# Performance work log

Measured on AMD Instinct MI355X. Metric: run time of the kernel, lower is better.

Reference implementation:

```python
import jax, jax.numpy as jnp
import numpy as np

DIM_QK = 1024


def setup_inputs() -> dict:
    key = jax.random.key(0)
    ks = jax.random.split(key, 5)
    B, S, D = 4, 2048, 1024
    return {
        "x": jax.random.normal(ks[0], (B, S, D), dtype=jnp.float32),
        "Wq": jax.random.normal(ks[1], (DIM_QK, D), dtype=jnp.float32) * (D ** -0.5),
        "Wk": jax.random.normal(ks[2], (DIM_QK, D), dtype=jnp.float32) * (D ** -0.5),
        "Wv": jax.random.normal(ks[3], (D, D), dtype=jnp.float32) * (D ** -0.5),
        "Wo": jax.random.normal(ks[4], (D, D), dtype=jnp.float32) * (D ** -0.5),
    }


def reference(x, Wq, Wk, Wv, Wo):
    # torch Linear: y = x @ W.T (no bias)
    q = jnp.einsum('bsd,kd->bsk', x, Wq)
    k = jnp.einsum('bsd,kd->bsk', x, Wk)
    v = jnp.einsum('bsd,vd->bsv', x, Wv)
    scale = (DIM_QK // 2) ** (-0.5)
    dist = jnp.einsum('bqk,btk->bqt', q, k) * scale  # [B,S,S]
    weight = jax.lax.stop_gradient(dist)             # pre-softmax scores (detached)
    attn = jax.nn.softmax(dist, axis=-1)
    ctx = jnp.einsum('bqt,btv->bqv', attn, v)
    out = jnp.einsum('bqv,ev->bqe', ctx, Wo)
    return (out, weight)
```

## Files before the change

kernel.cpp:

```cpp
#include <hip/hip_runtime.h>
#include <stdint.h>

typedef __attribute__((ext_vector_type(8))) short bf16x8;
typedef __attribute__((ext_vector_type(4))) float f32x4;

__device__ __forceinline__ unsigned short f32_to_bf16(float f) {
  union { float f; unsigned int u; } v; v.f = f;
  unsigned int u = v.u;
  u += 0x7fffu + ((u >> 16) & 1u);
  return (unsigned short)(u >> 16);
}

__device__ __forceinline__ void gload_lds16(const unsigned short* g, unsigned short* lds) {
  __builtin_amdgcn_global_load_lds(
      (const __attribute__((address_space(1))) unsigned int*)g,
      (__attribute__((address_space(3))) unsigned int*)lds,
      16, 0, 0);
}

template<int MODE>
__global__ __launch_bounds__(256, 2)
void gemm_bt(const unsigned short* __restrict__ A,
             const unsigned short* __restrict__ Bm,
             void* __restrict__ Cv,
             int M, int N, int K, int lda, int ldb, int ldc,
             long sA_, long sB_, long sC_,
             float scale)
{
  __shared__ unsigned short sA[2 * 128 * 32];
  __shared__ unsigned short sB[2 * 128 * 32];

  const int bz = blockIdx.z;
  const unsigned short* Ab = A + (long)bz * sA_;
  const unsigned short* Bb = Bm + (long)bz * sB_;

  const int m0 = blockIdx.x * 128;
  const int n0 = blockIdx.y * 128;

  const int t = threadIdx.x;
  const int lane = t & 63;
  const int w = t >> 6;
  const int wr = (w >> 1) * 64;
  const int wc = (w & 1) * 64;

  f32x4 acc[4][4];
#pragma unroll
  for (int i = 0; i < 4; ++i)
#pragma unroll
    for (int j = 0; j < 4; ++j)
      acc[i][j] = (f32x4){0.f, 0.f, 0.f, 0.f};

  const int r0 = t >> 2;
  const int kc = (t & 3) * 8;
  const unsigned short* Ap0 = Ab + (long)(m0 + r0) * lda + kc;
  const unsigned short* Ap1 = Ab + (long)(m0 + r0 + 64) * lda + kc;
  const unsigned short* Bp0 = Bb + (long)(n0 + r0) * ldb + kc;
  const unsigned short* Bp1 = Bb + (long)(n0 + r0 + 64) * ldb + kc;

  const int lrow = lane & 15;
  const int q8 = (lane >> 4) * 8;

  for (int k0 = 0; k0 < K; k0 += 64) {
    __syncthreads();
    gload_lds16(Ap0 + k0,      &sA[t * 8]);
    gload_lds16(Ap1 + k0,      &sA[t * 8 + 2048]);
    gload_lds16(Ap0 + k0 + 32, &sA[4096 + t * 8]);
    gload_lds16(Ap1 + k0 + 32, &sA[4096 + t * 8 + 2048]);
    gload_lds16(Bp0 + k0,      &sB[t * 8]);
    gload_lds16(Bp1 + k0,      &sB[t * 8 + 2048]);
    gload_lds16(Bp0 + k0 + 32, &sB[4096 + t * 8]);
    gload_lds16(Bp1 + k0 + 32, &sB[4096 + t * 8 + 2048]);
    __syncthreads();

#pragma unroll
    for (int s = 0; s < 2; ++s) {
      bf16x8 af[4], bfr[4];
#pragma unroll
      for (int i = 0; i < 4; ++i) {
        af[i]  = *(const bf16x8*)&sA[s * 4096 + (wr + i * 16 + lrow) * 32 + q8];
        bfr[i] = *(const bf16x8*)&sB[s * 4096 + (wc + i * 16 + lrow) * 32 + q8];
      }
#pragma unroll
      for (int mi = 0; mi < 4; ++mi)
#pragma unroll
        for (int ni = 0; ni < 4; ++ni)
          acc[mi][ni] = __builtin_amdgcn_mfma_f32_16x16x32_bf16(af[mi], bfr[ni], acc[mi][ni], 0, 0, 0);
    }
  }

  const int cl = lane & 15;
  const int rq = (lane >> 4) * 4;

  if (MODE == 2) {
    float* Cb = (float*)Cv + (long)bz * sC_;
#pragma unroll
    for (int mi = 0; mi < 4; ++mi) {
      const int rowb = m0 + wr + mi * 16 + rq;
#pragma unroll
      for (int ni = 0; ni < 4; ++ni) {
        const int col = n0 + wc + ni * 16 + cl;
#pragma unroll
        for (int r = 0; r < 4; ++r)
          Cb[(long)(rowb + r) * ldc + col] = acc[mi][ni][r] * scale;
      }
    }
  } else {
    unsigned short* Cb = (unsigned short*)Cv + (long)bz * sC_;
#pragma unroll
    for (int mi = 0; mi < 4; ++mi) {
      const int rowb = m0 + wr + mi * 16 + rq;
#pragma unroll
      for (int ni = 0; ni < 4; ++ni) {
        const int col = n0 + wc + ni * 16 + cl;
#pragma unroll
        for (int r = 0; r < 4; ++r)
          Cb[(long)(rowb + r) * ldc + col] = f32_to_bf16(acc[mi][ni][r]);
      }
    }
  }
}

__global__ __launch_bounds__(256)
void softmax_rows(const float* __restrict__ dist, unsigned short* __restrict__ attn) {
  const long row = blockIdx.x;
  const float4* in = (const float4*)(dist + row * 2048);
  const int t = threadIdx.x;
  float4 v0 = in[t];
  float4 v1 = in[t + 256];

  float m = fmaxf(fmaxf(fmaxf(v0.x, v0.y), fmaxf(v0.z, v0.w)),
                  fmaxf(fmaxf(v1.x, v1.y), fmaxf(v1.z, v1.w)));
#pragma unroll
  for (int off = 32; off > 0; off >>= 1)
    m = fmaxf(m, __shfl_xor(m, off, 64));

  __shared__ float redm[4];
  __shared__ float reds[4];
  if ((t & 63) == 0) redm[t >> 6] = m;
  __syncthreads();
  m = fmaxf(fmaxf(redm[0], redm[1]), fmaxf(redm[2], redm[3]));

  float e[8];
  e[0] = __expf(v0.x - m); e[1] = __expf(v0.y - m);
  e[2] = __expf(v0.z - m); e[3] = __expf(v0.w - m);
  e[4] = __expf(v1.x - m); e[5] = __expf(v1.y - m);
  e[6] = __expf(v1.z - m); e[7] = __expf(v1.w - m);

  float s = ((e[0] + e[1]) + (e[2] + e[3])) + ((e[4] + e[5]) + (e[6] + e[7]));
#pragma unroll
  for (int off = 32; off > 0; off >>= 1)
    s += __shfl_xor(s, off, 64);
  if ((t & 63) == 0) reds[t >> 6] = s;
  __syncthreads();
  s = (reds[0] + reds[1]) + (reds[2] + reds[3]);

  const float inv = 1.0f / s;
  ushort4 o0, o1;
  o0.x = f32_to_bf16(e[0] * inv); o0.y = f32_to_bf16(e[1] * inv);
  o0.z = f32_to_bf16(e[2] * inv); o0.w = f32_to_bf16(e[3] * inv);
  o1.x = f32_to_bf16(e[4] * inv); o1.y = f32_to_bf16(e[5] * inv);
  o1.z = f32_to_bf16(e[6] * inv); o1.w = f32_to_bf16(e[7] * inv);
  *(ushort4*)(attn + row * 2048 + t * 4) = o0;
  *(ushort4*)(attn + row * 2048 + 1024 + t * 4) = o1;
}

__global__ __launch_bounds__(256)
void cast_all(const float* __restrict__ Wq, const float* __restrict__ Wk,
              const float* __restrict__ Wv, const float* __restrict__ Wo,
              const float* __restrict__ x, unsigned short* __restrict__ dst) {
  const long i = ((long)blockIdx.x * 256 + threadIdx.x) * 4;
  const float* src;
  long off;
  if (i < 4194304) {
    const int which = (int)(i >> 20);
    src = (which == 0) ? Wq : (which == 1) ? Wk : (which == 2) ? Wv : Wo;
    off = i & 1048575;
  } else {
    src = x;
    off = i - 4194304;
  }
  float4 v = *(const float4*)(src + off);
  ushort4 o;
  o.x = f32_to_bf16(v.x); o.y = f32_to_bf16(v.y);
  o.z = f32_to_bf16(v.z); o.w = f32_to_bf16(v.w);
  *(ushort4*)(dst + i) = o;
}

extern "C" void kernel_launch(void* const* d_in, const int* in_sizes, int n_in,
                              void* d_out, int out_size, void* d_ws, size_t ws_size,
                              hipStream_t stream) {
  const float* x  = (const float*)d_in[0];
  const float* Wq = (const float*)d_in[1];
  const float* Wk = (const float*)d_in[2];
  const float* Wv = (const float*)d_in[3];
  const float* Wo = (const float*)d_in[4];

  const long Bn = 4, S = 2048, D = 1024;
  const long MS = Bn * S;

  float* out_p  = (float*)d_out;
  float* weight = out_p + MS * D;

  unsigned short* Wqb = (unsigned short*)d_ws;
  unsigned short* Wvb = Wqb + 2 * D * D;
  unsigned short* Wob = Wvb + D * D;
  unsigned short* xb  = Wob + D * D;
  unsigned short* qk  = xb + MS * D;
  unsigned short* vtb = qk + MS * 2048;
  unsigned short* attn = qk;
  unsigned short* ctx  = xb;

  cast_all<<<12288, 256, 0, stream>>>(Wq, Wk, Wv, Wo, x, Wqb);

  gemm_bt<0><<<dim3(64, 16, 1), 256, 0, stream>>>(xb, Wqb, qk, 8192, 2048, 1024,
                                                  1024, 1024, 2048, 0, 0, 0, 1.f);
  gemm_bt<0><<<dim3(8, 16, 4), 256, 0, stream>>>(Wvb, xb, vtb, 1024, 2048, 1024,
                                                 1024, 1024, 2048, 0, S * D, D * S, 1.f);
  gemm_bt<2><<<dim3(16, 16, 4), 256, 0, stream>>>(qk, qk + 1024, weight, 2048, 2048, 1024,
                                                  2048, 2048, 2048,
                                                  S * 2048, S * 2048, S * S,
                                                  0.04419417382415922f);
  softmax_rows<<<(int)(Bn * S), 256, 0, stream>>>(weight, attn);
  gemm_bt<0><<<dim3(16, 8, 4), 256, 0, stream>>>(attn, vtb, ctx, 2048, 1024, 2048,
                                                 2048, 2048, 1024,
                                                 S * S, D * S, S * D, 1.f);
  gemm_bt<2><<<dim3(64, 8, 1), 256, 0, stream>>>(ctx, Wob, out_p, 8192, 1024, 1024,
                                                 1024, 1024, 1024, 0, 0, 0, 1.f);
}
```

Before: 319.7 us.

## Rewrite GEMM as 256x256-tile, 512-thread kernel with software-pipelined LDS prefetch

Replaces the 128x128 double-sync GEMM with a 256x256 tile computed by 8 waves. Global-to-LDS loads for the next k-tiles are issued in the middle of the MFMA phases across a 128KB double buffer, with explicit vmcnt waits and raised wave priority around the MFMAs. The larger tiles improve operand reuse, and the prefetch is meant to hide load latency behind compute. In exchange, the large LDS footprint and 32 accumulators per lane reduce occupancy, and some GEMMs now launch only 128-256 blocks.

```diff
diff --git a/kernel.cpp b/kernel.cpp
--- a/kernel.cpp
+++ b/kernel.cpp
@@ -11,15 +11,63 @@
   return (unsigned short)(u >> 16);
 }
 
-__device__ __forceinline__ void gload_lds16(const unsigned short* g, unsigned short* lds) {
+__device__ __forceinline__ void gload_lds16(const unsigned short* g, unsigned short* lds_p) {
   __builtin_amdgcn_global_load_lds(
       (const __attribute__((address_space(1))) unsigned int*)g,
-      (__attribute__((address_space(3))) unsigned int*)lds,
+      (__attribute__((address_space(3))) unsigned int*)lds_p,
       16, 0, 0);
 }
 
+
+#define VM8  asm volatile("s_waitcnt vmcnt(8)" ::: "memory")
+#define VM4  asm volatile("s_waitcnt vmcnt(4)" ::: "memory")
+#define VM0_ asm volatile("s_waitcnt vmcnt(0)" ::: "memory")
+#define VMNO ((void)0)
+
+#define ISSUE_A(KT, KK) do {                                                  \
+    const unsigned short* ga_ = As0 + (KT) * 64 + (KK) * 32;                  \
+    unsigned short* la_ = &lds[(((KT) & 1) << 15) + (KK) * 8192 + t * 8];     \
+    gload_lds16(ga_, la_);                                                    \
+    gload_lds16(ga_ + a128, la_ + 4096);                                      \
+  } while (0)
+
+#define ISSUE_B(KT, KK) do {                                                  \
+    const unsigned short* gb_ = Bs0 + (KT) * 64 + (KK) * 32;                  \
+    unsigned short* lb_ = &lds[(((KT) & 1) << 15) + 16384 + (KK) * 8192 + t * 8]; \
+    gload_lds16(gb_, lb_);                                                    \
+    gload_lds16(gb_ + b128, lb_ + 4096);                                      \
+  } while (0)
+
+#define PH(BUFB, KK, MH, LOADB, ISSUE_CODE, VMC) do {                         \
+    const int ab_ = (BUFB) + (KK) * 8192;                                     \
+    if (LOADB) {                                                              \
+      const int bb2_ = (BUFB) + 16384 + (KK) * 8192;                          \
+      _Pragma("unroll")                                                       \
+      for (int ni_ = 0; ni_ < 4; ++ni_)                                       \
+        bfr[ni_] = *(const bf16x8*)&lds[bb2_ + (wc + ni_ * 16 + lrow) * 32 + q8e]; \
+    }                                                                         \
+    bf16x8 af_[4];                                                            \
+    _Pragma("unroll")                                                         \
+    for (int mi_ = 0; mi_ < 4; ++mi_)                                         \
+      af_[mi_] = *(const bf16x8*)&lds[ab_ + (wr + (MH) * 64 + mi_ * 16 + lrow) * 32 + q8e]; \
+    ISSUE_CODE;                                                               \
+    __builtin_amdgcn_s_setprio(1);                                            \
+    _Pragma("unroll")                                                         \
+    for (int mi_ = 0; mi_ < 4; ++mi_) {                                       \
+      _Pragma("unroll")                                                       \
+      for (int ni_ = 0; ni_ < 4; ++ni_)                                       \
+        acc[(MH) * 4 + mi_][ni_] = __builtin_amdgcn_mfma_f32_16x16x32_bf16(   \
+            af_[mi_], bfr[ni_], acc[(MH) * 4 + mi_][ni_], 0, 0, 0);           \
+    }                                                                         \
+    __builtin_amdgcn_s_setprio(0);                                            \
+    VMC;                                                                      \
+    asm volatile("s_waitcnt lgkmcnt(0)" ::: "memory");                        \
+    __builtin_amdgcn_s_barrier();                                             \
+    asm volatile("" ::: "memory");                                            \
+  } while (0)
+
 template<int MODE>
-__global__ __launch_bounds__(256, 2)
+__global__ __launch_bounds__(512, 2)
 void gemm_bt(const unsigned short* __restrict__ A,
              const unsigned short* __restrict__ Bm,
              void* __restrict__ Cv,
@@ -27,65 +75,69 @@
              long sA_, long sB_, long sC_,
              float scale)
 {
-  __shared__ unsigned short sA[2 * 128 * 32];
-  __shared__ unsigned short sB[2 * 128 * 32];
+  __shared__ unsigned short lds[65536];
 
   const int bz = blockIdx.z;
   const unsigned short* Ab = A + (long)bz * sA_;
   const unsigned short* Bb = Bm + (long)bz * sB_;
 
-  const int m0 = blockIdx.x * 128;
-  const int n0 = blockIdx.y * 128;
+  const int m0 = blockIdx.x * 256;
+  const int n0 = blockIdx.y * 256;
 
   const int t = threadIdx.x;
   const int lane = t & 63;
   const int w = t >> 6;
-  const int wr = (w >> 1) * 64;
-  const int wc = (w & 1) * 64;
-
-  f32x4 acc[4][4];
-#pragma unroll
-  for (int i = 0; i < 4; ++i)
+  const int wr = (w >> 2) * 128;
+  const int wc = (w & 3) * 64;
+  const int lrow = lane & 15;
+  const int q8e = (lane >> 4) * 8;
+
+  const int row0 = t >> 2;
+  const int kc0 = (t & 3) * 8;
+  const unsigned short* As0 = Ab + (long)(m0 + row0) * lda + kc0;
+  const unsigned short* Bs0 = Bb + (long)(n0 + row0) * ldb + kc0;
+  const long a128 = (long)lda * 128;
+  const long b128 = (long)ldb * 128;
+
+  f32x4 acc[8][4];
+#pragma unroll
+  for (int i = 0; i < 8; ++i)
 #pragma unroll
     for (int j = 0; j < 4; ++j)
       acc[i][j] = (f32x4){0.f, 0.f, 0.f, 0.f};
 
-  const int r0 = t >> 2;
-  const int kc = (t & 3) * 8;
-  const unsigned short* Ap0 = Ab + (long)(m0 + r0) * lda + kc;
-  const unsigned short* Ap1 = Ab + (long)(m0 + r0 + 64) * lda + kc;
-  const unsigned short* Bp0 = Bb + (long)(n0 + r0) * ldb + kc;
-  const unsigned short* Bp1 = Bb + (long)(n0 + r0 + 64) * ldb + kc;
-
-  const int lrow = lane & 15;
-  const int q8 = (lane >> 4) * 8;
-
-  for (int k0 = 0; k0 < K; k0 += 64) {
-    __syncthreads();
-    gload_lds16(Ap0 + k0,      &sA[t * 8]);
-    gload_lds16(Ap1 + k0,      &sA[t * 8 + 2048]);
-    gload_lds16(Ap0 + k0 + 32, &sA[4096 + t * 8]);
-    gload_lds16(Ap1 + k0 + 32, &sA[4096 + t * 8 + 2048]);
-    gload_lds16(Bp0 + k0,      &sB[t * 8]);
-    gload_lds16(Bp1 + k0,      &sB[t * 8 + 2048]);
-    gload_lds16(Bp0 + k0 + 32, &sB[4096 + t * 8]);
-    gload_lds16(Bp1 + k0 + 32, &sB[4096 + t * 8 + 2048]);
-    __syncthreads();
-
-#pragma unroll
-    for (int s = 0; s < 2; ++s) {
-      bf16x8 af[4], bfr[4];
-#pragma unroll
-      for (int i = 0; i < 4; ++i) {
-        af[i]  = *(const bf16x8*)&sA[s * 4096 + (wr + i * 16 + lrow) * 32 + q8];
-        bfr[i] = *(const bf16x8*)&sB[s * 4096 + (wc + i * 16 + lrow) * 32 + q8];
-      }
-#pragma unroll
-      for (int mi = 0; mi < 4; ++mi)
-#pragma unroll
-        for (int ni = 0; ni < 4; ++ni)
-          acc[mi][ni] = __builtin_amdgcn_mfma_f32_16x16x32_bf16(af[mi], bfr[ni], acc[mi][ni], 0, 0, 0);
-    }
+  const int NT = K >> 6;
+
+  ISSUE_A(0, 0); ISSUE_B(0, 0);
+  ISSUE_A(0, 1); ISSUE_B(0, 1);
+  ISSUE_A(1, 0); ISSUE_B(1, 0);
+  VM8;
+  __builtin_amdgcn_s_barrier();
+  asm volatile("" ::: "memory");
+
+  bf16x8 bfr[4];
+  int kt = 0;
+  for (; kt < NT - 2; ++kt) {
+    const int bb = (kt & 1) << 15;
+    PH(bb, 0, 0, 1, ISSUE_A(kt + 1, 1), VMNO);
+    PH(bb, 0, 1, 0, ISSUE_B(kt + 1, 1), VM8);
+    PH(bb, 1, 0, 1, ISSUE_A(kt + 2, 0), VMNO);
+    PH(bb, 1, 1, 0, ISSUE_B(kt + 2, 0), VM8);
+  }
+  {
+    const int bb = (kt & 1) << 15;
+    PH(bb, 0, 0, 1, ISSUE_A(kt + 1, 1), VMNO);
+    PH(bb, 0, 1, 0, ISSUE_B(kt + 1, 1), VM8);
+    PH(bb, 1, 0, 1, VMNO, VMNO);
+    PH(bb, 1, 1, 0, VMNO, VM4);
+    ++kt;
+  }
+  {
+    const int bb = (kt & 1) << 15;
+    PH(bb, 0, 0, 1, VMNO, VMNO);
+    PH(bb, 0, 1, 0, VMNO, VM0_);
+    PH(bb, 1, 0, 1, VMNO, VMNO);
+    PH(bb, 1, 1, 0, VMNO, VMNO);
   }
 
   const int cl = lane & 15;
@@ -94,27 +146,27 @@
   if (MODE == 2) {
     float* Cb = (float*)Cv + (long)bz * sC_;
 #pragma unroll
-    for (int mi = 0; mi < 4; ++mi) {
-      const int rowb = m0 + wr + mi * 16 + rq;
+    for (int mig = 0; mig < 8; ++mig) {
+      const int rowb = m0 + wr + (mig >> 2) * 64 + (mig & 3) * 16 + rq;
 #pragma unroll
       for (int ni = 0; ni < 4; ++ni) {
         const int col = n0 + wc + ni * 16 + cl;
 #pragma unroll
         for (int r = 0; r < 4; ++r)
-          Cb[(long)(rowb + r) * ldc + col] = acc[mi][ni][r] * scale;
+          Cb[(long)(rowb + r) * ldc + col] = acc[mig][ni][r] * scale;
       }
     }
   } else {
     unsigned short* Cb = (unsigned short*)Cv + (long)bz * sC_;
 #pragma unroll
-    for (int mi = 0; mi < 4; ++mi) {
-      const int rowb = m0 + wr + mi * 16 + rq;
+    for (int mig = 0; mig < 8; ++mig) {
+      const int rowb = m0 + wr + (mig >> 2) * 64 + (mig & 3) * 16 + rq;
 #pragma unroll
       for (int ni = 0; ni < 4; ++ni) {
         const int col = n0 + wc + ni * 16 + cl;
 #pragma unroll
         for (int r = 0; r < 4; ++r)
-          Cb[(long)(rowb + r) * ldc + col] = f32_to_bf16(acc[mi][ni][r]);
+          Cb[(long)(rowb + r) * ldc + col] = f32_to_bf16(acc[mig][ni][r]);
       }
     }
   }
@@ -212,18 +264,18 @@
 
   cast_all<<<12288, 256, 0, stream>>>(Wq, Wk, Wv, Wo, x, Wqb);
 
-  gemm_bt<0><<<dim3(64, 16, 1), 256, 0, stream>>>(xb, Wqb, qk, 8192, 2048, 1024,
-                                                  1024, 1024, 2048, 0, 0, 0, 1.f);
-  gemm_bt<0><<<dim3(8, 16, 4), 256, 0, stream>>>(Wvb, xb, vtb, 1024, 2048, 1024,
-                                                 1024, 1024, 2048, 0, S * D, D * S, 1.f);
-  gemm_bt<2><<<dim3(16, 16, 4), 256, 0, stream>>>(qk, qk + 1024, weight, 2048, 2048, 1024,
-                                                  2048, 2048, 2048,
-                                                  S * 2048, S * 2048, S * S,
-                                                  0.04419417382415922f);
+  gemm_bt<0><<<dim3(32, 8, 1), 512, 0, stream>>>(xb, Wqb, qk, 8192, 2048, 1024,
+                                                 1024, 1024, 2048, 0, 0, 0, 1.f);
+  gemm_bt<0><<<dim3(4, 8, 4), 512, 0, stream>>>(Wvb, xb, vtb, 1024, 2048, 1024,
+                                                1024, 1024, 2048, 0, S * D, D * S, 1.f);
+  gemm_bt<2><<<dim3(8, 8, 4), 512, 0, stream>>>(qk, qk + 1024, weight, 2048, 2048, 1024,
+                                                2048, 2048, 2048,
+                                                S * 2048, S * 2048, S * S,
+                                                0.04419417382415922f);
   softmax_rows<<<(int)(Bn * S), 256, 0, stream>>>(weight, attn);
-  gemm_bt<0><<<dim3(16, 8, 4), 256, 0, stream>>>(attn, vtb, ctx, 2048, 1024, 2048,
-                                                 2048, 2048, 1024,
-                                                 S * S, D * S, S * D, 1.f);
-  gemm_bt<2><<<dim3(64, 8, 1), 256, 0, stream>>>(ctx, Wob, out_p, 8192, 1024, 1024,
+  gemm_bt<0><<<dim3(8, 4, 4), 512, 0, stream>>>(attn, vtb, ctx, 2048, 1024, 2048,
+                                                2048, 2048, 1024,
+                                                S * S, D * S, S * D, 1.f);
+  gemm_bt<2><<<dim3(32, 4, 1), 512, 0, stream>>>(ctx, Wob, out_p, 8192, 1024, 1024,
                                                  1024, 1024, 1024, 0, 0, 0, 1.f);
 }
```

After: 346.9 us. 8.5% more time.

## Swizzle LDS tiles, add 128x256 GEMM tile, merge V projection into one GEMM

Applied to the files above, without the earlier changes.

Stores the A and B tiles in LDS with an XOR-swizzled k-chunk index (row-dependent), and reads them back with the matching swizzle. The aim is to cut bank conflicts on the 16-byte fragment reads feeding the MFMAs. A new gemm_a kernel with a 128x256 block tile and 4x8 accumulators per wave is used for the Q/K projection and the QK^T score GEMM, raising operand reuse per LDS load at the cost of more accumulator registers and fewer blocks. The V^T projection becomes a single non-batched GEMM producing a 1024x8192 layout, and the attn@V GEMM reads it with an adjusted stride.

```diff
diff --git a/kernel.cpp b/kernel.cpp
--- a/kernel.cpp
+++ b/kernel.cpp
@@ -11,21 +11,125 @@
   return (unsigned short)(u >> 16);
 }
 
-__device__ __forceinline__ void gload_lds16(const unsigned short* g, unsigned short* lds) {
+__device__ __forceinline__ void gload_lds16(const unsigned short* g, unsigned short* lds_p) {
   __builtin_amdgcn_global_load_lds(
       (const __attribute__((address_space(1))) unsigned int*)g,
-      (__attribute__((address_space(3))) unsigned int*)lds,
+      (__attribute__((address_space(3))) unsigned int*)lds_p,
       16, 0, 0);
 }
+
 
 template<int MODE>
 __global__ __launch_bounds__(256, 2)
-void gemm_bt(const unsigned short* __restrict__ A,
-             const unsigned short* __restrict__ Bm,
-             void* __restrict__ Cv,
-             int M, int N, int K, int lda, int ldb, int ldc,
-             long sA_, long sB_, long sC_,
-             float scale)
+void gemm_a(const unsigned short* __restrict__ A,
+            const unsigned short* __restrict__ Bm,
+            void* __restrict__ Cv,
+            int M, int N, int K, int lda, int ldb, int ldc,
+            long sA_, long sB_, long sC_,
+            float scale)
+{
+  __shared__ unsigned short sA[2 * 128 * 32];
+  __shared__ unsigned short sB[2 * 256 * 32];
+
+  const int bz = blockIdx.z;
+  const unsigned short* Ab = A + (long)bz * sA_;
+  const unsigned short* Bb = Bm + (long)bz * sB_;
+
+  const int m0 = blockIdx.x * 128;
+  const int n0 = blockIdx.y * 256;
+
+  const int t = threadIdx.x;
+  const int lane = t & 63;
+  const int w = t >> 6;
+  const int wr = (w >> 1) * 64;
+  const int wc = (w & 1) * 128;
+  const int lrow = lane & 15;
+  const int q8s = ((lane >> 4) ^ ((lrow >> 1) & 3)) * 8;
+
+  const int row0 = t >> 2;
+  const int kc0 = ((t & 3) ^ ((t >> 3) & 3)) * 8;
+  const unsigned short* Ap = Ab + (long)(m0 + row0) * lda + kc0;
+  const unsigned short* Bp = Bb + (long)(n0 + row0) * ldb + kc0;
+  const long a64 = (long)lda * 64;
+  const long b64 = (long)ldb * 64;
+
+  f32x4 acc[4][8];
+#pragma unroll
+  for (int i = 0; i < 4; ++i)
+#pragma unroll
+    for (int j = 0; j < 8; ++j)
+      acc[i][j] = (f32x4){0.f, 0.f, 0.f, 0.f};
+
+  for (int k0 = 0; k0 < K; k0 += 64) {
+    __syncthreads();
+#pragma unroll
+    for (int s = 0; s < 2; ++s) {
+      const int gk = k0 + s * 32;
+      gload_lds16(Ap + gk,       &sA[s * 4096 + t * 8]);
+      gload_lds16(Ap + a64 + gk, &sA[s * 4096 + t * 8 + 2048]);
+#pragma unroll
+      for (int j = 0; j < 4; ++j)
+        gload_lds16(Bp + j * b64 + gk, &sB[s * 8192 + t * 8 + j * 2048]);
+    }
+    __syncthreads();
+
+#pragma unroll
+    for (int s = 0; s < 2; ++s) {
+      bf16x8 af[4], bf[8];
+#pragma unroll
+      for (int i = 0; i < 4; ++i)
+        af[i] = *(const bf16x8*)&sA[s * 4096 + (wr + i * 16 + lrow) * 32 + q8s];
+#pragma unroll
+      for (int n = 0; n < 8; ++n)
+        bf[n] = *(const bf16x8*)&sB[s * 8192 + (wc + n * 16 + lrow) * 32 + q8s];
+#pragma unroll
+      for (int mi = 0; mi < 4; ++mi)
+#pragma unroll
+        for (int ni = 0; ni < 8; ++ni)
+          acc[mi][ni] = __builtin_amdgcn_mfma_f32_16x16x32_bf16(af[mi], bf[ni], acc[mi][ni], 0, 0, 0);
+    }
+  }
+
+  const int cl = lane & 15;
+  const int rq = (lane >> 4) * 4;
+
+  if (MODE == 2) {
+    float* Cb = (float*)Cv + (long)bz * sC_;
+#pragma unroll
+    for (int mi = 0; mi < 4; ++mi) {
+      const int rowb = m0 + wr + mi * 16 + rq;
+#pragma unroll
+      for (int ni = 0; ni < 8; ++ni) {
+        const int col = n0 + wc + ni * 16 + cl;
+#pragma unroll
+        for (int r = 0; r < 4; ++r)
+          Cb[(long)(rowb + r) * ldc + col] = acc[mi][ni][r] * scale;
+      }
+    }
+  } else {
+    unsigned short* Cb = (unsigned short*)Cv + (long)bz * sC_;
+#pragma unroll
+    for (int mi = 0; mi < 4; ++mi) {
+      const int rowb = m0 + wr + mi * 16 + rq;
+#pragma unroll
+      for (int ni = 0; ni < 8; ++ni) {
+        const int col = n0 + wc + ni * 16 + cl;
+#pragma unroll
+        for (int r = 0; r < 4; ++r)
+          Cb[(long)(rowb + r) * ldc + col] = f32_to_bf16(acc[mi][ni][r]);
+      }
+    }
+  }
+}
+
+template<int MODE>
+__global__ __launch_bounds__(256, 2)
+void gemm_b(const unsigned short* __restrict__ A,
+            const unsigned short* __restrict__ Bm,
+            void* __restrict__ Cv,
+            int M, int N, int K, int lda, int ldb, int ldc,
+            long sA_, long sB_, long sC_,
+            float scale)
 {
   __shared__ unsigned short sA[2 * 128 * 32];
   __shared__ unsigned short sB[2 * 128 * 32];
@@ -42,6 +146,15 @@
   const int w = t >> 6;
   const int wr = (w >> 1) * 64;
   const int wc = (w & 1) * 64;
+  const int lrow = lane & 15;
+  const int q8s = ((lane >> 4) ^ ((lrow >> 1) & 3)) * 8;
+
+  const int row0 = t >> 2;
+  const int kc0 = ((t & 3) ^ ((t >> 3) & 3)) * 8;
+  const unsigned short* Ap = Ab + (long)(m0 + row0) * lda + kc0;
+  const unsigned short* Bp = Bb + (long)(n0 + row0) * ldb + kc0;
+  const long a64 = (long)lda * 64;
+  const long b64 = (long)ldb * 64;
 
   f32x4 acc[4][4];
 #pragma unroll
@@ -50,41 +163,31 @@
     for (int j = 0; j < 4; ++j)
       acc[i][j] = (f32x4){0.f, 0.f, 0.f, 0.f};
 
-  const int r0 = t >> 2;
-  const int kc = (t & 3) * 8;
-  const unsigned short* Ap0 = Ab + (long)(m0 + r0) * lda + kc;
-  const unsigned short* Ap1 = Ab + (long)(m0 + r0 + 64) * lda + kc;
-  const unsigned short* Bp0 = Bb + (long)(n0 + r0) * ldb + kc;
-  const unsigned short* Bp1 = Bb + (long)(n0 + r0 + 64) * ldb + kc;
-
-  const int lrow = lane & 15;
-  const int q8 = (lane >> 4) * 8;
-
   for (int k0 = 0; k0 < K; k0 += 64) {
     __syncthreads();
-    gload_lds16(Ap0 + k0,      &sA[t * 8]);
-    gload_lds16(Ap1 + k0,      &sA[t * 8 + 2048]);
-    gload_lds16(Ap0 + k0 + 32, &sA[4096 + t * 8]);
-    gload_lds16(Ap1 + k0 + 32, &sA[4096 + t * 8 + 2048]);
-    gload_lds16(Bp0 + k0,      &sB[t * 8]);
-    gload_lds16(Bp1 + k0,      &sB[t * 8 + 2048]);
-    gload_lds16(Bp0 + k0 + 32, &sB[4096 + t * 8]);
-    gload_lds16(Bp1 + k0 + 32, &sB[4096 + t * 8 + 2048]);
+#pragma unroll
+    for (int s = 0; s < 2; ++s) {
+      const int gk = k0 + s * 32;
+      gload_lds16(Ap + gk,       &sA[s * 4096 + t * 8]);
+      gload_lds16(Ap + a64 + gk, &sA[s * 4096 + t * 8 + 2048]);
+      gload_lds16(Bp + gk,       &sB[s * 4096 + t * 8]);
+      gload_lds16(Bp + b64 + gk, &sB[s * 4096 + t * 8 + 2048]);
+    }
     __syncthreads();
 
 #pragma unroll
     for (int s = 0; s < 2; ++s) {
-      bf16x8 af[4], bfr[4];
+      bf16x8 af[4], bf[4];
 #pragma unroll
       for (int i = 0; i < 4; ++i) {
-        af[i]  = *(const bf16x8*)&sA[s * 4096 + (wr + i * 16 + lrow) * 32 + q8];
-        bfr[i] = *(const bf16x8*)&sB[s * 4096 + (wc + i * 16 + lrow) * 32 + q8];
+        af[i] = *(const bf16x8*)&sA[s * 4096 + (wr + i * 16 + lrow) * 32 + q8s];
+        bf[i] = *(const bf16x8*)&sB[s * 4096 + (wc + i * 16 + lrow) * 32 + q8s];
       }
 #pragma unroll
       for (int mi = 0; mi < 4; ++mi)
 #pragma unroll
         for (int ni = 0; ni < 4; ++ni)
-          acc[mi][ni] = __builtin_amdgcn_mfma_f32_16x16x32_bf16(af[mi], bfr[ni], acc[mi][ni], 0, 0, 0);
+          acc[mi][ni] = __builtin_amdgcn_mfma_f32_16x16x32_bf16(af[mi], bf[ni], acc[mi][ni], 0, 0, 0);
     }
   }
 
@@ -212,18 +315,18 @@
 
   cast_all<<<12288, 256, 0, stream>>>(Wq, Wk, Wv, Wo, x, Wqb);
 
-  gemm_bt<0><<<dim3(64, 16, 1), 256, 0, stream>>>(xb, Wqb, qk, 8192, 2048, 1024,
-                                                  1024, 1024, 2048, 0, 0, 0, 1.f);
-  gemm_bt<0><<<dim3(8, 16, 4), 256, 0, stream>>>(Wvb, xb, vtb, 1024, 2048, 1024,
-                                                 1024, 1024, 2048, 0, S * D, D * S, 1.f);
-  gemm_bt<2><<<dim3(16, 16, 4), 256, 0, stream>>>(qk, qk + 1024, weight, 2048, 2048, 1024,
-                                                  2048, 2048, 2048,
-                                                  S * 2048, S * 2048, S * S,
-                                                  0.04419417382415922f);
+  gemm_a<0><<<dim3(64, 8, 1), 256, 0, stream>>>(xb, Wqb, qk, 8192, 2048, 1024,
+                                                1024, 1024, 2048, 0, 0, 0, 1.f);
+  gemm_b<0><<<dim3(8, 64, 1), 256, 0, stream>>>(Wvb, xb, vtb, 1024, 8192, 1024,
+                                                1024, 1024, 8192, 0, 0, 0, 1.f);
+  gemm_a<2><<<dim3(16, 8, 4), 256, 0, stream>>>(qk, qk + 1024, weight, 2048, 2048, 1024,
+                                                2048, 2048, 2048,
+                                                S * 2048, S * 2048, S * S,
+                                                0.04419417382415922f);
   softmax_rows<<<(int)(Bn * S), 256, 0, stream>>>(weight, attn);
-  gemm_bt<0><<<dim3(16, 8, 4), 256, 0, stream>>>(attn, vtb, ctx, 2048, 1024, 2048,
-                                                 2048, 2048, 1024,
-                                                 S * S, D * S, S * D, 1.f);
-  gemm_bt<2><<<dim3(64, 8, 1), 256, 0, stream>>>(ctx, Wob, out_p, 8192, 1024, 1024,
-                                                 1024, 1024, 1024, 0, 0, 0, 1.f);
-}
+  gemm_b<0><<<dim3(16, 8, 4), 256, 0, stream>>>(attn, vtb, ctx, 2048, 1024, 2048,
+                                                2048, 8192, 1024,
+                                                S * S, 2048, S * D, 1.f);
+  gemm_b<2><<<dim3(64, 8, 1), 256, 0, stream>>>(ctx, Wob, out_p, 8192, 1024, 1024,
+                                                1024, 1024, 1024, 0, 0, 0, 1.f);
+}
```

Result: no change. 319.9 us (+0.1%).

## Swizzle LDS layout, remap workgroups across XCDs, raise occupancy, flatten V GEMM

Applied to the files above, without the earlier changes.

The GEMM now XOR-swizzles the 8-element k-chunk position in LDS, on both the global-to-LDS store and the fragment reads, to cut LDS bank conflicts. It also remaps the flat workgroup index so that consecutive tiles are grouped per XCD (stride of eight) for better L2 locality. Launch bounds ask for 4 waves per SIMD instead of 2, which may force register spills given the 64 accumulator floats per thread. The V projection becomes a single unbatched GEMM over all 8192 tokens, with a transposed V layout of leading dimension 8192, and the attention-times-V call is given the matching strides.

```diff
diff --git a/kernel.cpp b/kernel.cpp
--- a/kernel.cpp
+++ b/kernel.cpp
@@ -11,15 +11,15 @@
   return (unsigned short)(u >> 16);
 }
 
-__device__ __forceinline__ void gload_lds16(const unsigned short* g, unsigned short* lds) {
+__device__ __forceinline__ void gload_lds16(const unsigned short* g, unsigned short* lds_p) {
   __builtin_amdgcn_global_load_lds(
       (const __attribute__((address_space(1))) unsigned int*)g,
-      (__attribute__((address_space(3))) unsigned int*)lds,
+      (__attribute__((address_space(3))) unsigned int*)lds_p,
       16, 0, 0);
 }
 
 template<int MODE>
-__global__ __launch_bounds__(256, 2)
+__global__ __launch_bounds__(256, 4)
 void gemm_bt(const unsigned short* __restrict__ A,
              const unsigned short* __restrict__ Bm,
              void* __restrict__ Cv,
@@ -34,14 +34,28 @@
   const unsigned short* Ab = A + (long)bz * sA_;
   const unsigned short* Bb = Bm + (long)bz * sB_;
 
-  const int m0 = blockIdx.x * 128;
-  const int n0 = blockIdx.y * 128;
+  const int nx = gridDim.x;
+  const int nwg = nx * gridDim.y;
+  const int f = blockIdx.y * nx + blockIdx.x;
+  const int cpx = nwg >> 3;
+  const int sw = (f & 7) * cpx + (f >> 3);
+  const int m0 = (sw % nx) * 128;
+  const int n0 = (sw / nx) * 128;
 
   const int t = threadIdx.x;
   const int lane = t & 63;
   const int w = t >> 6;
   const int wr = (w >> 1) * 64;
   const int wc = (w & 1) * 64;
+  const int lrow = lane & 15;
+  const int q8s = ((lane >> 4) ^ ((lrow >> 1) & 3)) * 8;
+
+  const int row0 = t >> 2;
+  const int kc0 = ((t & 3) ^ ((t >> 3) & 3)) * 8;
+  const unsigned short* Ap = Ab + (long)(m0 + row0) * lda + kc0;
+  const unsigned short* Bp = Bb + (long)(n0 + row0) * ldb + kc0;
+  const long a64 = (long)lda * 64;
+  const long b64 = (long)ldb * 64;
 
   f32x4 acc[4][4];
 #pragma unroll
@@ -50,41 +64,31 @@
     for (int j = 0; j < 4; ++j)
       acc[i][j] = (f32x4){0.f, 0.f, 0.f, 0.f};
 
-  const int r0 = t >> 2;
-  const int kc = (t & 3) * 8;
-  const unsigned short* Ap0 = Ab + (long)(m0 + r0) * lda + kc;
-  const unsigned short* Ap1 = Ab + (long)(m0 + r0 + 64) * lda + kc;
-  const unsigned short* Bp0 = Bb + (long)(n0 + r0) * ldb + kc;
-  const unsigned short* Bp1 = Bb + (long)(n0 + r0 + 64) * ldb + kc;
-
-  const int lrow = lane & 15;
-  const int q8 = (lane >> 4) * 8;
-
   for (int k0 = 0; k0 < K; k0 += 64) {
     __syncthreads();
-    gload_lds16(Ap0 + k0,      &sA[t * 8]);
-    gload_lds16(Ap1 + k0,      &sA[t * 8 + 2048]);
-    gload_lds16(Ap0 + k0 + 32, &sA[4096 + t * 8]);
-    gload_lds16(Ap1 + k0 + 32, &sA[4096 + t * 8 + 2048]);
-    gload_lds16(Bp0 + k0,      &sB[t * 8]);
-    gload_lds16(Bp1 + k0,      &sB[t * 8 + 2048]);
-    gload_lds16(Bp0 + k0 + 32, &sB[4096 + t * 8]);
-    gload_lds16(Bp1 + k0 + 32, &sB[4096 + t * 8 + 2048]);
+#pragma unroll
+    for (int s = 0; s < 2; ++s) {
+      const int gk = k0 + s * 32;
+      gload_lds16(Ap + gk,       &sA[s * 4096 + t * 8]);
+      gload_lds16(Ap + a64 + gk, &sA[s * 4096 + t * 8 + 2048]);
+      gload_lds16(Bp + gk,       &sB[s * 4096 + t * 8]);
+      gload_lds16(Bp + b64 + gk, &sB[s * 4096 + t * 8 + 2048]);
+    }
     __syncthreads();
 
 #pragma unroll
     for (int s = 0; s < 2; ++s) {
-      bf16x8 af[4], bfr[4];
+      bf16x8 af[4], bf[4];
 #pragma unroll
       for (int i = 0; i < 4; ++i) {
-        af[i]  = *(const bf16x8*)&sA[s * 4096 + (wr + i * 16 + lrow) * 32 + q8];
-        bfr[i] = *(const bf16x8*)&sB[s * 4096 + (wc + i * 16 + lrow) * 32 + q8];
+        af[i] = *(const bf16x8*)&sA[s * 4096 + (wr + i * 16 + lrow) * 32 + q8s];
+        bf[i] = *(const bf16x8*)&sB[s * 4096 + (wc + i * 16 + lrow) * 32 + q8s];
       }
 #pragma unroll
       for (int mi = 0; mi < 4; ++mi)
 #pragma unroll
         for (int ni = 0; ni < 4; ++ni)
-          acc[mi][ni] = __builtin_amdgcn_mfma_f32_16x16x32_bf16(af[mi], bfr[ni], acc[mi][ni], 0, 0, 0);
+          acc[mi][ni] = __builtin_amdgcn_mfma_f32_16x16x32_bf16(af[mi], bf[ni], acc[mi][ni], 0, 0, 0);
     }
   }
 
@@ -214,16 +218,16 @@
 
   gemm_bt<0><<<dim3(64, 16, 1), 256, 0, stream>>>(xb, Wqb, qk, 8192, 2048, 1024,
                                                   1024, 1024, 2048, 0, 0, 0, 1.f);
-  gemm_bt<0><<<dim3(8, 16, 4), 256, 0, stream>>>(Wvb, xb, vtb, 1024, 2048, 1024,
-                                                 1024, 1024, 2048, 0, S * D, D * S, 1.f);
+  gemm_bt<0><<<dim3(8, 64, 1), 256, 0, stream>>>(Wvb, xb, vtb, 1024, 8192, 1024,
+                                                 1024, 1024, 8192, 0, 0, 0, 1.f);
   gemm_bt<2><<<dim3(16, 16, 4), 256, 0, stream>>>(qk, qk + 1024, weight, 2048, 2048, 1024,
                                                   2048, 2048, 2048,
                                                   S * 2048, S * 2048, S * S,
                                                   0.04419417382415922f);
   softmax_rows<<<(int)(Bn * S), 256, 0, stream>>>(weight, attn);
   gemm_bt<0><<<dim3(16, 8, 4), 256, 0, stream>>>(attn, vtb, ctx, 2048, 1024, 2048,
-                                                 2048, 2048, 1024,
-                                                 S * S, D * S, S * D, 1.f);
+                                                 2048, 8192, 1024,
+                                                 S * S, 2048, S * D, 1.f);
   gemm_bt<2><<<dim3(64, 8, 1), 256, 0, stream>>>(ctx, Wob, out_p, 8192, 1024, 1024,
                                                  1024, 1024, 1024, 0, 0, 0, 1.f);
 }
```

Result: slower. 333.9 us (+4.4%).
